# Optimization experiments

Measured on AMD Instinct MI355X. Metric: run time of the kernel, lower is better.

Reference implementation:

```python
import jax, jax.numpy as jnp
import numpy as np

B, T, C, E, TOPK = 4, 4096, 1024, 8, 2
H = 4 * C

def setup_inputs() -> dict:
    key = jax.random.key(0)
    ks = jax.random.split(key, 8)
    s = 1.0 / np.sqrt(C)
    sh = 1.0 / np.sqrt(H)
    return {
        "x": jax.random.normal(ks[0], (B, T, C), jnp.float32),
        "noise_eps": jax.random.normal(ks[1], (B, T, E), jnp.float32),
        "route_w": jax.random.normal(ks[2], (C, E), jnp.float32) * s,
        "route_b": jnp.zeros((E,), jnp.float32),
        "noise_w": jax.random.normal(ks[3], (C, E), jnp.float32) * s,
        "noise_b": jnp.zeros((E,), jnp.float32),
        "w1": jax.random.normal(ks[4], (E, C, H), jnp.float32) * s,
        "b1": jnp.zeros((E, H), jnp.float32),
        "w2": jax.random.normal(ks[5], (E, H, C), jnp.float32) * sh,
        "b2": jnp.zeros((E, C), jnp.float32),
        "top_k": TOPK,
    }

def reference(x, noise_eps, route_w, route_b, noise_w, noise_b, w1, b1, w2, b2, top_k):
    Bq, Tq, Cq = x.shape
    nE = route_w.shape[1]
    xf = x.reshape(Bq * Tq, Cq)                      # [N, C]
    N = xf.shape[0]
    logits = xf @ route_w + route_b                   # [N, E]
    std = jax.nn.softplus(xf @ noise_w + noise_b)     # [N, E]
    noisy = logits + noise_eps.reshape(N, nE) * std   # [N, E]
    _, top_idx = jax.lax.top_k(noisy, top_k)          # [N, K]
    rows = jnp.arange(N)[:, None]
    mask = jnp.zeros((N, nE), bool).at[rows, top_idx].set(True)
    # softmax over only the selected logits (others -> prob 0)
    probs = jax.nn.softmax(jnp.where(mask, noisy, -jnp.inf), axis=-1)  # [N, E]
    out = jnp.zeros_like(xf)
    for e in range(nE):  # small fixed expert count
        h = jax.nn.relu(xf @ w1[e] + b1[e])           # [N, 4C]
        y = h @ w2[e] + b2[e]                         # [N, C]
        out = out + probs[:, e:e + 1] * y             # prob==0 for unrouted tokens
    return out.reshape(Bq, Tq, Cq)
```

## Files before the change

### kernel.cpp

```cpp
#include <hip/hip_runtime.h>
#include <hip/hip_bf16.h>
#include <stdint.h>

#define NC 1024
#define NE 8
#define NH 4096
#define NN 16384

typedef __bf16 bf16x8_t __attribute__((ext_vector_type(8)));
typedef float f32x4_t __attribute__((ext_vector_type(4)));

__device__ __forceinline__ void cvt8(const float4 a, const float4 b, __bf16* dst) {
  bf16x8_t r;
  r[0] = (__bf16)a.x; r[1] = (__bf16)a.y; r[2] = (__bf16)a.z; r[3] = (__bf16)a.w;
  r[4] = (__bf16)b.x; r[5] = (__bf16)b.y; r[6] = (__bf16)b.z; r[7] = (__bf16)b.w;
  *(bf16x8_t*)dst = r;
}

__global__ __launch_bounds__(256) void routing_kernel(
    const float* __restrict__ x, const float* __restrict__ eps,
    const float* __restrict__ rw, const float* __restrict__ rb,
    const float* __restrict__ nw, const float* __restrict__ nb,
    int* __restrict__ eidx, float2* __restrict__ pp2) {
  const int lane = threadIdx.x & 63;
  const int n = blockIdx.x * 4 + (threadIdx.x >> 6);
  if (n >= NN) return;
  double acc[16];
#pragma unroll
  for (int i = 0; i < 16; ++i) acc[i] = 0.0;
  const float* xr = x + (size_t)n * NC;
  for (int c0 = 0; c0 < NC; c0 += 64) {
    const int c = c0 + lane;
    const float xv = xr[c];
    const float4 r0 = *(const float4*)(rw + (size_t)c * NE);
    const float4 r1 = *(const float4*)(rw + (size_t)c * NE + 4);
    const float4 n0 = *(const float4*)(nw + (size_t)c * NE);
    const float4 n1 = *(const float4*)(nw + (size_t)c * NE + 4);
    acc[0] += (double)xv * r0.x;  acc[1] += (double)xv * r0.y;
    acc[2] += (double)xv * r0.z;  acc[3] += (double)xv * r0.w;
    acc[4] += (double)xv * r1.x;  acc[5] += (double)xv * r1.y;
    acc[6] += (double)xv * r1.z;  acc[7] += (double)xv * r1.w;
    acc[8] += (double)xv * n0.x;  acc[9] += (double)xv * n0.y;
    acc[10] += (double)xv * n0.z; acc[11] += (double)xv * n0.w;
    acc[12] += (double)xv * n1.x; acc[13] += (double)xv * n1.y;
    acc[14] += (double)xv * n1.z; acc[15] += (double)xv * n1.w;
  }
#pragma unroll
  for (int off = 32; off > 0; off >>= 1) {
#pragma unroll
    for (int i = 0; i < 16; ++i) acc[i] += __shfl_xor(acc[i], off, 64);
  }
  if (lane == 0) {
    double noisy[NE];
#pragma unroll
    for (int e = 0; e < NE; ++e) {
      const double lg = acc[e] + (double)rb[e];
      const double z = acc[8 + e] + (double)nb[e];
      const double sp = log1p(exp(-fabs(z))) + fmax(z, 0.0);
      noisy[e] = lg + (double)eps[(size_t)n * NE + e] * sp;
    }
    int i1 = -1, i2 = -1;
    double v1 = -1e300, v2 = -1e300;
#pragma unroll
    for (int e = 0; e < NE; ++e) {
      const double v = noisy[e];
      if (v > v1) { v2 = v1; i2 = i1; v1 = v; i1 = e; }
      else if (v > v2) { v2 = v; i2 = e; }
    }
    if (i1 < 0) i1 = 0;
    if (i2 < 0 || i2 == i1) i2 = (i1 + 1) & 7;
    const double d = exp(v2 - v1);
    const float p1 = (float)(1.0 / (1.0 + d));
    const float p2 = (float)(d / (1.0 + d));
    eidx[n] = i1 | (i2 << 8);
    pp2[n] = float2{p1, p2};
  }
}

__global__ __launch_bounds__(256) void build_lists(
    const int* __restrict__ eidx, const float2* __restrict__ pp2,
    int* __restrict__ counts, int* __restrict__ perm, float* __restrict__ pprob) {
  __shared__ int hist[NE];
  __shared__ int base[NE];
  const int t = threadIdx.x;
  if (t < NE) hist[t] = 0;
  __syncthreads();
  const int n = blockIdx.x * 256 + t;
  const int packed = eidx[n];
  const int e1 = packed & 255;
  const int e2 = (packed >> 8) & 255;
  const float2 p = pp2[n];
  const int l1 = atomicAdd(&hist[e1], 1);
  const int l2 = atomicAdd(&hist[e2], 1);
  __syncthreads();
  if (t < NE) base[t] = atomicAdd(&counts[t], hist[t]);
  __syncthreads();
  const int o1 = base[e1] + l1;
  const int o2 = base[e2] + l2;
  perm[e1 * NN + o1] = n; pprob[e1 * NN + o1] = p.x;
  perm[e2 * NN + o2] = n; pprob[e2 * NN + o2] = p.y;
}

__global__ __launch_bounds__(256) void transpose_cvt(
    const float* __restrict__ src, __bf16* __restrict__ dst, int R, int Cc) {
  __shared__ __align__(16) __bf16 tile[64][72];
  const int r0 = blockIdx.y * 64, c0 = blockIdx.x * 64;
  const int t = threadIdx.x;
  const int tr = t >> 3;
  const int tc = (t & 7) * 8;
#pragma unroll
  for (int h = 0; h < 2; ++h) {
    const int r = tr + h * 32;
    const float* sp = src + (size_t)(r0 + r) * Cc + (c0 + tc);
    const float4 a = *(const float4*)sp;
    const float4 b = *(const float4*)(sp + 4);
    cvt8(a, b, &tile[r][tc]);
  }
  __syncthreads();
#pragma unroll
  for (int h = 0; h < 2; ++h) {
    const int c = tr + h * 32;
    __bf16 tmp[8] __attribute__((aligned(16)));
#pragma unroll
    for (int j = 0; j < 8; ++j) tmp[j] = tile[tc + j][c];
    __bf16* dp = dst + (size_t)(c0 + c) * R + (r0 + tc);
    *(uint4*)dp = *(const uint4*)tmp;
  }
}


template<bool FASTB>
__global__ __launch_bounds__(256) void moe_gemm1(
    const float* __restrict__ x, const void* __restrict__ bsrc,
    const float* __restrict__ bias, __bf16* __restrict__ hbuf,
    const int* __restrict__ counts_e, const int* __restrict__ perm_e, int chunk_start) {
  int cnt = *counts_e; if (cnt > NN) cnt = NN; if (cnt < 0) cnt = 0;
  const int lr0 = blockIdx.y * 128;
  const int row0 = chunk_start + lr0;
  if (row0 >= cnt) return;
  const int t = threadIdx.x;

  __shared__ __align__(16) __bf16 As[2 * 128 * 32];
  __shared__ __align__(16) __bf16 Bs[2 * 128 * 32];

  const int ar1 = row0 + (t >> 2), ar2 = ar1 + 64;
  const int tokA = (ar1 < cnt) ? perm_e[ar1] : 0;
  const int tokB = (ar2 < cnt) ? perm_e[ar2] : 0;
  const int kg = (t & 3) * 8;
  const float* pA1 = x + (size_t)tokA * NC + kg;
  const float* pA2 = x + (size_t)tokB * NC + kg;
  const int n0 = blockIdx.x * 128;

  const __bf16* pB1 = nullptr; const __bf16* pB2 = nullptr;
  const float* pBw = nullptr;
  const int kk = t >> 3, cc = (t & 7) * 16;
  if (FASTB) {
    const __bf16* bt = (const __bf16*)bsrc;
    const int nrow = n0 + (t >> 2);
    pB1 = bt + (size_t)nrow * NC + kg;
    pB2 = bt + (size_t)(nrow + 64) * NC + kg;
  } else {
    pBw = (const float*)bsrc + (size_t)kk * NH + n0 + cc;
  }

  f32x4_t acc[4][4];
#pragma unroll
  for (int i = 0; i < 4; ++i)
#pragma unroll
    for (int j = 0; j < 4; ++j)
#pragma unroll
      for (int k = 0; k < 4; ++k) acc[i][j][k] = 0.f;

  const int lane = t & 63, wid = t >> 6;
  const int wm = (wid >> 1) * 64, wn = (wid & 1) * 64;
  const int col16 = lane & 15, quad = lane >> 4;

  if (FASTB) {
    const int woff = (t >> 2) * 32 + (((t & 3) ^ ((t >> 3) & 3)) * 8);
    const int sel = (col16 >> 1) & 3;
    const int a_off = (wm + col16) * 32 + ((quad ^ sel) * 8);
    const int b_off = (wn + col16) * 32 + ((quad ^ sel) * 8);

    float4 a1a = *(const float4*)(pA1);
    float4 a1b = *(const float4*)(pA1 + 4);
    float4 a2a = *(const float4*)(pA2);
    float4 a2b = *(const float4*)(pA2 + 4);
    uint4 vb1 = *(const uint4*)(pB1);
    uint4 vb2 = *(const uint4*)(pB2);
    int cur = 0;
    for (int k0 = 0; k0 < NC; k0 += 32) {
      __bf16* Asc = As + cur * 4096;
      __bf16* Bsc = Bs + cur * 4096;
      cvt8(a1a, a1b, Asc + woff);
      cvt8(a2a, a2b, Asc + 2048 + woff);
      *(uint4*)(Bsc + woff) = vb1;
      *(uint4*)(Bsc + 2048 + woff) = vb2;
      if (k0 + 32 < NC) {
        a1a = *(const float4*)(pA1 + k0 + 32);
        a1b = *(const float4*)(pA1 + k0 + 36);
        a2a = *(const float4*)(pA2 + k0 + 32);
        a2b = *(const float4*)(pA2 + k0 + 36);
        vb1 = *(const uint4*)(pB1 + k0 + 32);
        vb2 = *(const uint4*)(pB2 + k0 + 32);
      }
      __syncthreads();
      bf16x8_t af[4], bfr[4];
#pragma unroll
      for (int mi = 0; mi < 4; ++mi) af[mi] = *(const bf16x8_t*)(Asc + a_off + mi * 512);
#pragma unroll
      for (int ni = 0; ni < 4; ++ni) bfr[ni] = *(const bf16x8_t*)(Bsc + b_off + ni * 512);
#pragma unroll
      for (int mi = 0; mi < 4; ++mi)
#pragma unroll
        for (int ni = 0; ni < 4; ++ni)
          acc[mi][ni] = __builtin_amdgcn_mfma_f32_16x16x32_bf16(af[mi], bfr[ni], acc[mi][ni], 0, 0, 0);
      cur ^= 1;
    }
  } else {
    const int a_off = (wm + col16) * 32 + quad * 8;
    for (int k0 = 0; k0 < NC; k0 += 32) {
      const float4 a1a = *(const float4*)(pA1 + k0);
      const float4 a1b = *(const float4*)(pA1 + k0 + 4);
      const float4 a2a = *(const float4*)(pA2 + k0);
      const float4 a2b = *(const float4*)(pA2 + k0 + 4);
      const float* pw = pBw + (size_t)k0 * NH;
      const float4 w0 = *(const float4*)pw;
      const float4 w1 = *(const float4*)(pw + 4);
      const float4 w2 = *(const float4*)(pw + 8);
      const float4 w3 = *(const float4*)(pw + 12);
      __syncthreads();
      cvt8(a1a, a1b, As + t * 8);
      cvt8(a2a, a2b, As + 2048 + t * 8);
      cvt8(w0, w1, Bs + kk * 128 + cc);
      cvt8(w2, w3, Bs + kk * 128 + cc + 8);
      __syncthreads();
      bf16x8_t af[4], bfr[4];
#pragma unroll
      for (int mi = 0; mi < 4; ++mi) af[mi] = *(const bf16x8_t*)(As + a_off + mi * 512);
#pragma unroll
      for (int ni = 0; ni < 4; ++ni) {
        const int bn = wn + ni * 16 + col16;
#pragma unroll
        for (int j = 0; j < 8; ++j) bfr[ni][j] = Bs[(quad * 8 + j) * 128 + bn];
      }
#pragma unroll
      for (int mi = 0; mi < 4; ++mi)
#pragma unroll
        for (int ni = 0; ni < 4; ++ni)
          acc[mi][ni] = __builtin_amdgcn_mfma_f32_16x16x32_bf16(af[mi], bfr[ni], acc[mi][ni], 0, 0, 0);
    }
  }

  const int colbase = n0 + wn + col16;
#pragma unroll
  for (int mi = 0; mi < 4; ++mi)
#pragma unroll
    for (int reg = 0; reg < 4; ++reg) {
      const int lr = lr0 + wm + mi * 16 + quad * 4 + reg;
      if (chunk_start + lr < cnt) {
        __bf16* hp = hbuf + (size_t)lr * NH + colbase;
#pragma unroll
        for (int ni = 0; ni < 4; ++ni) {
          const float v = acc[mi][ni][reg] + bias[colbase + ni * 16];
          hp[ni * 16] = (__bf16)fmaxf(v, 0.f);
        }
      }
    }
}

template<bool FASTB>
__global__ __launch_bounds__(256) void moe_gemm2(
    const __bf16* __restrict__ hbuf, const void* __restrict__ bsrc,
    const float* __restrict__ bias, float* __restrict__ out,
    const int* __restrict__ counts_e, const int* __restrict__ perm_e,
    const float* __restrict__ pprob_e, int chunk_start) {
  int cnt = *counts_e; if (cnt > NN) cnt = NN; if (cnt < 0) cnt = 0;
  const int lr0 = blockIdx.y * 128;
  if (chunk_start + lr0 >= cnt) return;
  const int t = threadIdx.x;

  __shared__ __align__(16) __bf16 As[2 * 128 * 32];
  __shared__ __align__(16) __bf16 Bs[2 * 128 * 32];

  const int lar1 = lr0 + (t >> 2);
  const int kg = (t & 3) * 8;
  const __bf16* pA1 = hbuf + (size_t)lar1 * NH + kg;
  const __bf16* pA2 = pA1 + (size_t)64 * NH;
  const int n0 = blockIdx.x * 128;

  const __bf16* pB1 = nullptr; const __bf16* pB2 = nullptr;
  const float* pBw = nullptr;
  const int kk = t >> 3, cc = (t & 7) * 16;
  if (FASTB) {
    const __bf16* bt = (const __bf16*)bsrc;
    const int nrow = n0 + (t >> 2);
    pB1 = bt + (size_t)nrow * NH + kg;
    pB2 = bt + (size_t)(nrow + 64) * NH + kg;
  } else {
    pBw = (const float*)bsrc + (size_t)kk * NC + n0 + cc;
  }

  f32x4_t acc[4][4];
#pragma unroll
  for (int i = 0; i < 4; ++i)
#pragma unroll
    for (int j = 0; j < 4; ++j)
#pragma unroll
      for (int k = 0; k < 4; ++k) acc[i][j][k] = 0.f;

  const int lane = t & 63, wid = t >> 6;
  const int wm = (wid >> 1) * 64, wn = (wid & 1) * 64;
  const int col16 = lane & 15, quad = lane >> 4;

  if (FASTB) {
    const int woff = (t >> 2) * 32 + (((t & 3) ^ ((t >> 3) & 3)) * 8);
    const int sel = (col16 >> 1) & 3;
    const int a_off = (wm + col16) * 32 + ((quad ^ sel) * 8);
    const int b_off = (wn + col16) * 32 + ((quad ^ sel) * 8);

    uint4 va1 = *(const uint4*)(pA1);
    uint4 va2 = *(const uint4*)(pA2);
    uint4 vb1 = *(const uint4*)(pB1);
    uint4 vb2 = *(const uint4*)(pB2);
    int cur = 0;
    for (int k0 = 0; k0 < NH; k0 += 32) {
      __bf16* Asc = As + cur * 4096;
      __bf16* Bsc = Bs + cur * 4096;
      *(uint4*)(Asc + woff) = va1;
      *(uint4*)(Asc + 2048 + woff) = va2;
      *(uint4*)(Bsc + woff) = vb1;
      *(uint4*)(Bsc + 2048 + woff) = vb2;
      if (k0 + 32 < NH) {
        va1 = *(const uint4*)(pA1 + k0 + 32);
        va2 = *(const uint4*)(pA2 + k0 + 32);
        vb1 = *(const uint4*)(pB1 + k0 + 32);
        vb2 = *(const uint4*)(pB2 + k0 + 32);
      }
      __syncthreads();
      bf16x8_t af[4], bfr[4];
#pragma unroll
      for (int mi = 0; mi < 4; ++mi) af[mi] = *(const bf16x8_t*)(Asc + a_off + mi * 512);
#pragma unroll
      for (int ni = 0; ni < 4; ++ni) bfr[ni] = *(const bf16x8_t*)(Bsc + b_off + ni * 512);
#pragma unroll
      for (int mi = 0; mi < 4; ++mi)
#pragma unroll
        for (int ni = 0; ni < 4; ++ni)
          acc[mi][ni] = __builtin_amdgcn_mfma_f32_16x16x32_bf16(af[mi], bfr[ni], acc[mi][ni], 0, 0, 0);
      cur ^= 1;
    }
  } else {
    const int a_off = (wm + col16) * 32 + quad * 8;
    for (int k0 = 0; k0 < NH; k0 += 32) {
      const uint4 va1 = *(const uint4*)(pA1 + k0);
      const uint4 va2 = *(const uint4*)(pA2 + k0);
      const float* pw = pBw + (size_t)k0 * NC;
      const float4 w0 = *(const float4*)pw;
      const float4 w1 = *(const float4*)(pw + 4);
      const float4 w2 = *(const float4*)(pw + 8);
      const float4 w3 = *(const float4*)(pw + 12);
      __syncthreads();
      *(uint4*)(As + t * 8) = va1;
      *(uint4*)(As + 2048 + t * 8) = va2;
      cvt8(w0, w1, Bs + kk * 128 + cc);
      cvt8(w2, w3, Bs + kk * 128 + cc + 8);
      __syncthreads();
      bf16x8_t af[4], bfr[4];
#pragma unroll
      for (int mi = 0; mi < 4; ++mi) af[mi] = *(const bf16x8_t*)(As + a_off + mi * 512);
#pragma unroll
      for (int ni = 0; ni < 4; ++ni) {
        const int bn = wn + ni * 16 + col16;
#pragma unroll
        for (int j = 0; j < 8; ++j) bfr[ni][j] = Bs[(quad * 8 + j) * 128 + bn];
      }
#pragma unroll
      for (int mi = 0; mi < 4; ++mi)
#pragma unroll
        for (int ni = 0; ni < 4; ++ni)
          acc[mi][ni] = __builtin_amdgcn_mfma_f32_16x16x32_bf16(af[mi], bfr[ni], acc[mi][ni], 0, 0, 0);
    }
  }

  const int colbase = n0 + wn + col16;
#pragma unroll
  for (int mi = 0; mi < 4; ++mi)
#pragma unroll
    for (int reg = 0; reg < 4; ++reg) {
      const int lr = lr0 + wm + mi * 16 + quad * 4 + reg;
      const int r = chunk_start + lr;
      if (r < cnt) {
        const int tok = perm_e[r];
        const float p = pprob_e[r];
        float* op = out + (size_t)tok * NC + colbase;
#pragma unroll
        for (int ni = 0; ni < 4; ++ni) {
          op[ni * 16] += (acc[mi][ni][reg] + bias[colbase + ni * 16]) * p;
        }
      }
    }
}

extern "C" void kernel_launch(void* const* d_in, const int* in_sizes, int n_in,
                              void* d_out, int out_size, void* d_ws, size_t ws_size,
                              hipStream_t stream) {
  (void)in_sizes; (void)n_in;
  const float* x   = (const float*)d_in[0];
  const float* eps = (const float*)d_in[1];
  const float* rw  = (const float*)d_in[2];
  const float* rb  = (const float*)d_in[3];
  const float* nw  = (const float*)d_in[4];
  const float* nb  = (const float*)d_in[5];
  const float* w1  = (const float*)d_in[6];
  const float* b1  = (const float*)d_in[7];
  const float* w2  = (const float*)d_in[8];
  const float* b2  = (const float*)d_in[9];
  float* out = (float*)d_out;

  char* wsb = (char*)d_ws;
  int* counts = (int*)wsb;
  int* perm = (int*)(wsb + 256);
  float* pprob = (float*)(wsb + 256 + (size_t)NE * NN * 4);
  int* eidx = (int*)(wsb + 256 + (size_t)NE * NN * 8);
  float2* pp2 = (float2*)(wsb + 256 + (size_t)NE * NN * 8 + (size_t)NN * 4);
  size_t off = 256 + (size_t)NE * NN * 8 + (size_t)NN * 12;

  const size_t wtile = (size_t)NC * NH * 2;
  const bool fast = ws_size >= off + 2 * wtile + (size_t)128 * NH * 2 + (1u << 20);
  __bf16* w1t = nullptr; __bf16* w2t = nullptr;
  if (fast) {
    w1t = (__bf16*)(wsb + off); off += wtile;
    w2t = (__bf16*)(wsb + off); off += wtile;
  }
  __bf16* hbuf = (__bf16*)(wsb + off);
  const size_t remain = (ws_size > off) ? (ws_size - off) : 0;
  long rows_cap = (long)(remain / ((size_t)NH * 2));
  rows_cap = (rows_cap / 128) * 128;
  if (rows_cap > NN) rows_cap = NN;
  if (rows_cap < 128) rows_cap = 128;

  hipMemsetAsync(counts, 0, 256, stream);
  hipMemsetAsync(d_out, 0, (size_t)out_size * 4, stream);

  routing_kernel<<<NN / 4, 256, 0, stream>>>(x, eps, rw, rb, nw, nb, eidx, pp2);
  build_lists<<<NN / 256, 256, 0, stream>>>(eidx, pp2, counts, perm, pprob);

  const int nchunks = (int)((NN + rows_cap - 1) / rows_cap);
  for (int e = 0; e < NE; ++e) {
    const float* w1e = w1 + (size_t)e * NC * NH;
    const float* w2e = w2 + (size_t)e * NH * NC;
    if (fast) {
      transpose_cvt<<<dim3(NH / 64, NC / 64), 256, 0, stream>>>(w1e, w1t, NC, NH);
      transpose_cvt<<<dim3(NC / 64, NH / 64), 256, 0, stream>>>(w2e, w2t, NH, NC);
    }
    for (int ch = 0; ch < nchunks; ++ch) {
      const int cs = ch * (int)rows_cap;
      if (fast) {
        moe_gemm1<true><<<dim3(NH / 128, (unsigned)(rows_cap / 128)), 256, 0, stream>>>(
            x, w1t, b1 + (size_t)e * NH, hbuf, counts + e, perm + (size_t)e * NN, cs);
        moe_gemm2<true><<<dim3(NC / 128, (unsigned)(rows_cap / 128)), 256, 0, stream>>>(
            hbuf, w2t, b2 + (size_t)e * NC, out, counts + e, perm + (size_t)e * NN,
            pprob + (size_t)e * NN, cs);
      } else {
        moe_gemm1<false><<<dim3(NH / 128, (unsigned)(rows_cap / 128)), 256, 0, stream>>>(
            x, w1e, b1 + (size_t)e * NH, hbuf, counts + e, perm + (size_t)e * NN, cs);
        moe_gemm2<false><<<dim3(NC / 128, (unsigned)(rows_cap / 128)), 256, 0, stream>>>(
            hbuf, w2e, b2 + (size_t)e * NC, out, counts + e, perm + (size_t)e * NN,
            pprob + (size_t)e * NN, cs);
      }
    }
  }
}
```

Baseline: 1.717 ms.

## Batch weight transposes across experts and unroll GEMM k-loop with two-stage prefetch

When the workspace is large enough, all experts' weights are transposed and converted to bf16 in two batched launches (using blockIdx.z) instead of two launches per expert. Both expert GEMM kernels now unroll the k-loop by two and keep register prefetches for two stages, using explicit ping-pong shared buffers. The aim is fewer small launches and more load latency hidden behind MFMA work. The cost is more workspace, higher register pressure, and extra wasted wrap-around loads at the loop tail.

```diff
diff --git a/kernel.cpp b/kernel.cpp
--- a/kernel.cpp
+++ b/kernel.cpp
@@ -15,6 +15,20 @@
   r[0] = (__bf16)a.x; r[1] = (__bf16)a.y; r[2] = (__bf16)a.z; r[3] = (__bf16)a.w;
   r[4] = (__bf16)b.x; r[5] = (__bf16)b.y; r[6] = (__bf16)b.z; r[7] = (__bf16)b.w;
   *(bf16x8_t*)dst = r;
+}
+
+__device__ __forceinline__ void mfma_step(const __bf16* __restrict__ Asc,
+    const __bf16* __restrict__ Bsc, int a_off, int b_off, f32x4_t (&acc)[4][4]) {
+  bf16x8_t af[4], bfr[4];
+#pragma unroll
+  for (int mi = 0; mi < 4; ++mi) af[mi] = *(const bf16x8_t*)(Asc + a_off + mi * 512);
+#pragma unroll
+  for (int ni = 0; ni < 4; ++ni) bfr[ni] = *(const bf16x8_t*)(Bsc + b_off + ni * 512);
+#pragma unroll
+  for (int mi = 0; mi < 4; ++mi)
+#pragma unroll
+    for (int ni = 0; ni < 4; ++ni)
+      acc[mi][ni] = __builtin_amdgcn_mfma_f32_16x16x32_bf16(af[mi], bfr[ni], acc[mi][ni], 0, 0, 0);
 }
 
 __global__ __launch_bounds__(256) void routing_kernel(
@@ -103,6 +117,9 @@
 
 __global__ __launch_bounds__(256) void transpose_cvt(
     const float* __restrict__ src, __bf16* __restrict__ dst, int R, int Cc) {
+  const size_t mat = (size_t)R * Cc;
+  src += (size_t)blockIdx.z * mat;
+  dst += (size_t)blockIdx.z * mat;
   __shared__ __align__(16) __bf16 tile[64][72];
   const int r0 = blockIdx.y * 64, c0 = blockIdx.x * 64;
   const int t = threadIdx.x;
@@ -180,41 +197,41 @@
     const int sel = (col16 >> 1) & 3;
     const int a_off = (wm + col16) * 32 + ((quad ^ sel) * 8);
     const int b_off = (wn + col16) * 32 + ((quad ^ sel) * 8);
-
-    float4 a1a = *(const float4*)(pA1);
-    float4 a1b = *(const float4*)(pA1 + 4);
-    float4 a2a = *(const float4*)(pA2);
-    float4 a2b = *(const float4*)(pA2 + 4);
-    uint4 vb1 = *(const uint4*)(pB1);
-    uint4 vb2 = *(const uint4*)(pB2);
-    int cur = 0;
-    for (int k0 = 0; k0 < NC; k0 += 32) {
-      __bf16* Asc = As + cur * 4096;
-      __bf16* Bsc = Bs + cur * 4096;
-      cvt8(a1a, a1b, Asc + woff);
-      cvt8(a2a, a2b, Asc + 2048 + woff);
-      *(uint4*)(Bsc + woff) = vb1;
-      *(uint4*)(Bsc + 2048 + woff) = vb2;
-      if (k0 + 32 < NC) {
-        a1a = *(const float4*)(pA1 + k0 + 32);
-        a1b = *(const float4*)(pA1 + k0 + 36);
-        a2a = *(const float4*)(pA2 + k0 + 32);
-        a2b = *(const float4*)(pA2 + k0 + 36);
-        vb1 = *(const uint4*)(pB1 + k0 + 32);
-        vb2 = *(const uint4*)(pB2 + k0 + 32);
-      }
-      __syncthreads();
-      bf16x8_t af[4], bfr[4];
-#pragma unroll
-      for (int mi = 0; mi < 4; ++mi) af[mi] = *(const bf16x8_t*)(Asc + a_off + mi * 512);
-#pragma unroll
-      for (int ni = 0; ni < 4; ++ni) bfr[ni] = *(const bf16x8_t*)(Bsc + b_off + ni * 512);
-#pragma unroll
-      for (int mi = 0; mi < 4; ++mi)
-#pragma unroll
-        for (int ni = 0; ni < 4; ++ni)
-          acc[mi][ni] = __builtin_amdgcn_mfma_f32_16x16x32_bf16(af[mi], bfr[ni], acc[mi][ni], 0, 0, 0);
-      cur ^= 1;
+    __bf16* As0 = As; __bf16* As1 = As + 4096;
+    __bf16* Bs0 = Bs; __bf16* Bs1 = Bs + 4096;
+
+    float4 a1a0 = *(const float4*)(pA1),      a1b0 = *(const float4*)(pA1 + 4);
+    float4 a2a0 = *(const float4*)(pA2),      a2b0 = *(const float4*)(pA2 + 4);
+    uint4  vb10 = *(const uint4*)(pB1),       vb20 = *(const uint4*)(pB2);
+    float4 a1a1 = *(const float4*)(pA1 + 32), a1b1 = *(const float4*)(pA1 + 36);
+    float4 a2a1 = *(const float4*)(pA2 + 32), a2b1 = *(const float4*)(pA2 + 36);
+    uint4  vb11 = *(const uint4*)(pB1 + 32),  vb21 = *(const uint4*)(pB2 + 32);
+
+    for (int k0 = 0; k0 < NC; k0 += 64) {
+      cvt8(a1a0, a1b0, As0 + woff);
+      cvt8(a2a0, a2b0, As0 + 2048 + woff);
+      *(uint4*)(Bs0 + woff) = vb10;
+      *(uint4*)(Bs0 + 2048 + woff) = vb20;
+      {
+        const int kn = (k0 + 64 < NC) ? k0 + 64 : 0;
+        a1a0 = *(const float4*)(pA1 + kn); a1b0 = *(const float4*)(pA1 + kn + 4);
+        a2a0 = *(const float4*)(pA2 + kn); a2b0 = *(const float4*)(pA2 + kn + 4);
+        vb10 = *(const uint4*)(pB1 + kn);  vb20 = *(const uint4*)(pB2 + kn);
+      }
+      __syncthreads();
+      mfma_step(As0, Bs0, a_off, b_off, acc);
+      cvt8(a1a1, a1b1, As1 + woff);
+      cvt8(a2a1, a2b1, As1 + 2048 + woff);
+      *(uint4*)(Bs1 + woff) = vb11;
+      *(uint4*)(Bs1 + 2048 + woff) = vb21;
+      {
+        const int kn = (k0 + 96 < NC) ? k0 + 96 : 0;
+        a1a1 = *(const float4*)(pA1 + kn); a1b1 = *(const float4*)(pA1 + kn + 4);
+        a2a1 = *(const float4*)(pA2 + kn); a2b1 = *(const float4*)(pA2 + kn + 4);
+        vb11 = *(const uint4*)(pB1 + kn);  vb21 = *(const uint4*)(pB2 + kn);
+      }
+      __syncthreads();
+      mfma_step(As1, Bs1, a_off, b_off, acc);
     }
   } else {
     const int a_off = (wm + col16) * 32 + quad * 8;
@@ -317,37 +334,37 @@
     const int sel = (col16 >> 1) & 3;
     const int a_off = (wm + col16) * 32 + ((quad ^ sel) * 8);
     const int b_off = (wn + col16) * 32 + ((quad ^ sel) * 8);
-
-    uint4 va1 = *(const uint4*)(pA1);
-    uint4 va2 = *(const uint4*)(pA2);
-    uint4 vb1 = *(const uint4*)(pB1);
-    uint4 vb2 = *(const uint4*)(pB2);
-    int cur = 0;
-    for (int k0 = 0; k0 < NH; k0 += 32) {
-      __bf16* Asc = As + cur * 4096;
-      __bf16* Bsc = Bs + cur * 4096;
-      *(uint4*)(Asc + woff) = va1;
-      *(uint4*)(Asc + 2048 + woff) = va2;
-      *(uint4*)(Bsc + woff) = vb1;
-      *(uint4*)(Bsc + 2048 + woff) = vb2;
-      if (k0 + 32 < NH) {
-        va1 = *(const uint4*)(pA1 + k0 + 32);
-        va2 = *(const uint4*)(pA2 + k0 + 32);
-        vb1 = *(const uint4*)(pB1 + k0 + 32);
-        vb2 = *(const uint4*)(pB2 + k0 + 32);
-      }
-      __syncthreads();
-      bf16x8_t af[4], bfr[4];
-#pragma unroll
-      for (int mi = 0; mi < 4; ++mi) af[mi] = *(const bf16x8_t*)(Asc + a_off + mi * 512);
-#pragma unroll
-      for (int ni = 0; ni < 4; ++ni) bfr[ni] = *(const bf16x8_t*)(Bsc + b_off + ni * 512);
-#pragma unroll
-      for (int mi = 0; mi < 4; ++mi)
-#pragma unroll
-        for (int ni = 0; ni < 4; ++ni)
-          acc[mi][ni] = __builtin_amdgcn_mfma_f32_16x16x32_bf16(af[mi], bfr[ni], acc[mi][ni], 0, 0, 0);
-      cur ^= 1;
+    __bf16* As0 = As; __bf16* As1 = As + 4096;
+    __bf16* Bs0 = Bs; __bf16* Bs1 = Bs + 4096;
+
+    uint4 va10 = *(const uint4*)(pA1),      va20 = *(const uint4*)(pA2);
+    uint4 vb10 = *(const uint4*)(pB1),      vb20 = *(const uint4*)(pB2);
+    uint4 va11 = *(const uint4*)(pA1 + 32), va21 = *(const uint4*)(pA2 + 32);
+    uint4 vb11 = *(const uint4*)(pB1 + 32), vb21 = *(const uint4*)(pB2 + 32);
+
+    for (int k0 = 0; k0 < NH; k0 += 64) {
+      *(uint4*)(As0 + woff) = va10;
+      *(uint4*)(As0 + 2048 + woff) = va20;
+      *(uint4*)(Bs0 + woff) = vb10;
+      *(uint4*)(Bs0 + 2048 + woff) = vb20;
+      {
+        const int kn = (k0 + 64 < NH) ? k0 + 64 : 0;
+        va10 = *(const uint4*)(pA1 + kn); va20 = *(const uint4*)(pA2 + kn);
+        vb10 = *(const uint4*)(pB1 + kn); vb20 = *(const uint4*)(pB2 + kn);
+      }
+      __syncthreads();
+      mfma_step(As0, Bs0, a_off, b_off, acc);
+      *(uint4*)(As1 + woff) = va11;
+      *(uint4*)(As1 + 2048 + woff) = va21;
+      *(uint4*)(Bs1 + woff) = vb11;
+      *(uint4*)(Bs1 + 2048 + woff) = vb21;
+      {
+        const int kn = (k0 + 96 < NH) ? k0 + 96 : 0;
+        va11 = *(const uint4*)(pA1 + kn); va21 = *(const uint4*)(pA2 + kn);
+        vb11 = *(const uint4*)(pB1 + kn); vb21 = *(const uint4*)(pB2 + kn);
+      }
+      __syncthreads();
+      mfma_step(As1, Bs1, a_off, b_off, acc);
     }
   } else {
     const int a_off = (wm + col16) * 32 + quad * 8;
@@ -426,9 +443,15 @@
   size_t off = 256 + (size_t)NE * NN * 8 + (size_t)NN * 12;
 
   const size_t wtile = (size_t)NC * NH * 2;
-  const bool fast = ws_size >= off + 2 * wtile + (size_t)128 * NH * 2 + (1u << 20);
+  const size_t hfull = (size_t)NN * NH * 2;
+  const bool fast2 = ws_size >= off + 2 * NE * wtile + hfull + (4u << 20);
+  const bool fast = fast2 ||
+      ws_size >= off + 2 * wtile + (size_t)128 * NH * 2 + (1u << 20);
   __bf16* w1t = nullptr; __bf16* w2t = nullptr;
-  if (fast) {
+  if (fast2) {
+    w1t = (__bf16*)(wsb + off); off += NE * wtile;
+    w2t = (__bf16*)(wsb + off); off += NE * wtile;
+  } else if (fast) {
     w1t = (__bf16*)(wsb + off); off += wtile;
     w2t = (__bf16*)(wsb + off); off += wtile;
   }
@@ -445,21 +468,28 @@
   routing_kernel<<<NN / 4, 256, 0, stream>>>(x, eps, rw, rb, nw, nb, eidx, pp2);
   build_lists<<<NN / 256, 256, 0, stream>>>(eidx, pp2, counts, perm, pprob);
 
+  if (fast2) {
+    transpose_cvt<<<dim3(NH / 64, NC / 64, NE), 256, 0, stream>>>(w1, w1t, NC, NH);
+    transpose_cvt<<<dim3(NC / 64, NH / 64, NE), 256, 0, stream>>>(w2, w2t, NH, NC);
+  }
+
   const int nchunks = (int)((NN + rows_cap - 1) / rows_cap);
   for (int e = 0; e < NE; ++e) {
     const float* w1e = w1 + (size_t)e * NC * NH;
     const float* w2e = w2 + (size_t)e * NH * NC;
-    if (fast) {
-      transpose_cvt<<<dim3(NH / 64, NC / 64), 256, 0, stream>>>(w1e, w1t, NC, NH);
-      transpose_cvt<<<dim3(NC / 64, NH / 64), 256, 0, stream>>>(w2e, w2t, NH, NC);
+    const __bf16* w1te = fast2 ? (w1t + (size_t)e * NC * NH) : w1t;
+    const __bf16* w2te = fast2 ? (w2t + (size_t)e * NH * NC) : w2t;
+    if (fast && !fast2) {
+      transpose_cvt<<<dim3(NH / 64, NC / 64, 1), 256, 0, stream>>>(w1e, w1t, NC, NH);
+      transpose_cvt<<<dim3(NC / 64, NH / 64, 1), 256, 0, stream>>>(w2e, w2t, NH, NC);
     }
     for (int ch = 0; ch < nchunks; ++ch) {
       const int cs = ch * (int)rows_cap;
       if (fast) {
         moe_gemm1<true><<<dim3(NH / 128, (unsigned)(rows_cap / 128)), 256, 0, stream>>>(
-            x, w1t, b1 + (size_t)e * NH, hbuf, counts + e, perm + (size_t)e * NN, cs);
+            x, w1te, b1 + (size_t)e * NH, hbuf, counts + e, perm + (size_t)e * NN, cs);
         moe_gemm2<true><<<dim3(NC / 128, (unsigned)(rows_cap / 128)), 256, 0, stream>>>(
-            hbuf, w2t, b2 + (size_t)e * NC, out, counts + e, perm + (size_t)e * NN,
+            hbuf, w2te, b2 + (size_t)e * NC, out, counts + e, perm + (size_t)e * NN,
             pprob + (size_t)e * NN, cs);
       } else {
         moe_gemm1<false><<<dim3(NH / 128, (unsigned)(rows_cap / 128)), 256, 0, stream>>>(
```

Measured after the change: 1.659 ms. 1.04x faster.
